# Optimization experiments

Measured on AMD Instinct MI355X. Metric: run time of the kernel, lower is better.

## Reference

```python
import jax, jax.numpy as jnp
import numpy as np


def setup_inputs() -> dict:
    key = jax.random.key(0)
    k0, k1, k2, k3, k4 = jax.random.split(key, 5)
    N, C, H, W, K = 16, 256, 32, 32, 4096
    inv = 1.0 / np.sqrt(C).astype(np.float32)
    latent = jax.random.normal(k0, (N, C, H, W), jnp.float32)
    codebook = jax.random.normal(k1, (K, C), jnp.float32) * inv
    wq = jax.random.normal(k2, (C, C), jnp.float32) * inv
    wk = jax.random.normal(k3, (C, C), jnp.float32) * inv
    wv = jax.random.normal(k4, (C, C), jnp.float32) * inv
    return {"latent": latent, "codebook": codebook, "wq": wq, "wk": wk, "wv": wv, "temperature": 1}


def reference(latent, codebook, wq, wk, wv, temperature):
    # deterministic=True, additionWeight=True, dropout=False
    # temperature >= 0 -> _gumbelAttention -> _softStraightThrough path
    assert temperature >= 0
    C = latent.shape[1]
    K = codebook.shape[0]
    scale = jnp.sqrt(jnp.asarray(C, jnp.float32))
    x = jnp.transpose(latent, (0, 2, 3, 1))          # [N,H,W,C]
    q = x @ wq.T                                      # nn.Linear: x @ W^T
    k = codebook @ wk.T                               # [K,C]
    v = codebook @ wv.T                               # [K,C]
    logit = jnp.einsum('nhwc,kc->nhwk', q, k) / scale  # [N,H,W,K]
    soft = jax.nn.softmax(logit, axis=-1)
    idx = jnp.argmax(logit, axis=-1)                  # [N,H,W]
    hard = jax.nn.one_hot(idx, K, dtype=jnp.float32)  # [N,H,W,K]
    soft_v = jnp.einsum('nhwk,kc->nhwc', soft, v)
    hard_v = jnp.einsum('nhwk,kc->nhwc', hard, v)
    # (hard - soft).detach() + soft  -> straight-through estimator
    result = jax.lax.stop_gradient(hard_v - soft_v) + soft_v
    quantized = jnp.transpose(result, (0, 3, 1, 2))   # [N,C,H,W]
    code = idx.astype(jnp.uint8)                      # sample.argmax(-1).byte()
    return (quantized, code, logit, v)
```

## Files before the change

### kernel.cpp

```cpp
#include <hip/hip_runtime.h>
#include <stdint.h>

typedef float f32x4 __attribute__((ext_vector_type(4)));
typedef short s16x8 __attribute__((ext_vector_type(8)));

#define QUANT_OFF 0
#define CODE_OFF  4194304
#define LOGIT_OFF 4210688
#define V_OFF     71319552

#define ARGMAX_MARGIN 0.0078125f

__device__ __forceinline__ unsigned short f2bf(float f) {
  unsigned int u = __float_as_uint(f);
  u = u + 0x7fffu + ((u >> 16) & 1u);
  return (unsigned short)(u >> 16);
}

__device__ __forceinline__ void load_lds16(const void* g, void* l) {
  __builtin_amdgcn_global_load_lds(
      (const __attribute__((address_space(1))) unsigned int*)g,
      (__attribute__((address_space(3))) unsigned int*)l, 16, 0, 0);
}

__global__ __launch_bounds__(256) void kvq_kernel(
    const float* __restrict__ latent, const float* __restrict__ wq,
    const float* __restrict__ cb, const float* __restrict__ wk, const float* __restrict__ wv,
    float* __restrict__ qf, unsigned short* __restrict__ qh,
    float* __restrict__ kf, unsigned short* __restrict__ kh, float* __restrict__ vout)
{
  __shared__ __align__(16) float A_s[2][2048];
  __shared__ __align__(16) float B_s[2][2048];
  const int t = threadIdx.x;
  const int bid = blockIdx.x;
  const int tx = t & 15;
  const int ry = t >> 4;

  if (bid >= 512) {
    const int qb = bid - 512;
    const int rowBase = (qb & 255) * 64;
    const int colBase = (qb >> 8) * 64;
    const int n = rowBase >> 10;
    const int hw0 = rowBase & 1023;
    float acc[4][4] = {{0.f}};

    #define QSTAGE(B, KT) do {                                                        \
      _Pragma("unroll")                                                               \
      for (int it = 0; it < 2; ++it) {                                                \
        int c = it * 256 + t;                                                         \
        int kk = c >> 4, rq = c & 15;                                                 \
        load_lds16(latent + ((size_t)(n * 256 + (KT) * 32 + kk) * 1024 + hw0 + rq * 4), \
                   &A_s[B][c * 4]);                                                   \
        int col = c >> 3, ls = c & 7;                                                 \
        int sk = ls ^ (col & 7);                                                      \
        load_lds16(wq + ((size_t)(colBase + col) * 256 + (KT) * 32 + sk * 4),          \
                   &B_s[B][c * 4]);                                                   \
      } } while (0)

    QSTAGE(0, 0);
    #pragma unroll 1
    for (int kt = 0; kt < 8; ++kt) {
      const int buf = kt & 1;
      __syncthreads();
      if (kt < 7) QSTAGE(buf ^ 1, kt + 1);
      const float* As = A_s[buf];
      const float* Bs = B_s[buf];
      #pragma unroll
      for (int kc = 0; kc < 8; ++kc) {
        f32x4 a[4], b[4];
        #pragma unroll
        for (int c = 0; c < 4; ++c) a[c] = *(const f32x4*)&As[(kc * 4 + c) * 64 + ry * 4];
        #pragma unroll
        for (int j = 0; j < 4; ++j) {
          const int col = tx + 16 * j;
          b[j] = *(const f32x4*)&Bs[col * 32 + (kc ^ (col & 7)) * 4];
        }
        #pragma unroll
        for (int i = 0; i < 4; ++i)
          #pragma unroll
          for (int j = 0; j < 4; ++j) {
            acc[i][j] = fmaf(a[0][i], b[j].x, acc[i][j]);
            acc[i][j] = fmaf(a[1][i], b[j].y, acc[i][j]);
            acc[i][j] = fmaf(a[2][i], b[j].z, acc[i][j]);
            acc[i][j] = fmaf(a[3][i], b[j].w, acc[i][j]);
          }
      }
    }
    #undef QSTAGE
    #pragma unroll
    for (int i = 0; i < 4; ++i) {
      const int r = rowBase + ry * 4 + i;
      #pragma unroll
      for (int j = 0; j < 4; ++j) {
        const int c = colBase + tx + 16 * j;
        qf[(size_t)r * 256 + c] = acc[i][j];
        qh[(size_t)r * 256 + c] = f2bf(acc[i][j] * 0.0625f);
      }
    }
  } else {
    const bool isV = bid >= 256;
    const int kb = bid & 255;
    const int rowBase = (kb & 63) * 64;
    const int colBase = (kb >> 6) * 64;
    const float* W = isV ? wv : wk;
    float acc[4][4] = {{0.f}};

    #define KSTAGE(B, KT) do {                                                        \
      _Pragma("unroll")                                                               \
      for (int it = 0; it < 2; ++it) {                                                \
        int c = it * 256 + t;                                                         \
        int row = c >> 3, ls = c & 7;                                                 \
        int sk = ls ^ (row & 7);                                                      \
        load_lds16(cb + ((size_t)(rowBase + row) * 256 + (KT) * 32 + sk * 4),          \
                   &A_s[B][c * 4]);                                                   \
        load_lds16(W  + ((size_t)(colBase + row) * 256 + (KT) * 32 + sk * 4),          \
                   &B_s[B][c * 4]);                                                   \
      } } while (0)

    KSTAGE(0, 0);
    #pragma unroll 1
    for (int kt = 0; kt < 8; ++kt) {
      const int buf = kt & 1;
      __syncthreads();
      if (kt < 7) KSTAGE(buf ^ 1, kt + 1);
      const float* As = A_s[buf];
      const float* Bs = B_s[buf];
      #pragma unroll
      for (int kc = 0; kc < 8; ++kc) {
        f32x4 a[4], b[4];
        #pragma unroll
        for (int i = 0; i < 4; ++i) {
          const int row = ry + 16 * i;
          a[i] = *(const f32x4*)&As[row * 32 + (kc ^ (row & 7)) * 4];
        }
        #pragma unroll
        for (int j = 0; j < 4; ++j) {
          const int col = tx + 16 * j;
          b[j] = *(const f32x4*)&Bs[col * 32 + (kc ^ (col & 7)) * 4];
        }
        #pragma unroll
        for (int i = 0; i < 4; ++i)
          #pragma unroll
          for (int j = 0; j < 4; ++j) {
            acc[i][j] = fmaf(a[i].x, b[j].x, acc[i][j]);
            acc[i][j] = fmaf(a[i].y, b[j].y, acc[i][j]);
            acc[i][j] = fmaf(a[i].z, b[j].z, acc[i][j]);
            acc[i][j] = fmaf(a[i].w, b[j].w, acc[i][j]);
          }
      }
    }
    #undef KSTAGE
    #pragma unroll
    for (int i = 0; i < 4; ++i) {
      const int r = rowBase + ry + 16 * i;
      #pragma unroll
      for (int j = 0; j < 4; ++j) {
        const int c = colBase + tx + 16 * j;
        if (isV) {
          vout[(size_t)r * 256 + c] = acc[i][j];
        } else {
          kf[(size_t)r * 256 + c] = acc[i][j];
          kh[(size_t)r * 256 + c] = f2bf(acc[i][j]);
        }
      }
    }
  }
}

__global__ __launch_bounds__(256) void logit_gemm(
    const unsigned short* __restrict__ qh, const unsigned short* __restrict__ kh,
    float* __restrict__ out, float* __restrict__ pmax)
{
  __shared__ short AsBuf[2][128 * 32];
  __shared__ short BsBuf[2][128 * 32];
  __shared__ float Pm[128][2];
  const int t = threadIdx.x;
  const int bid = blockIdx.x;
  const int wg = (bid & 7) * 512 + (bid >> 3);
  const int aRow0 = (wg >> 5) * 128;
  const int bRow0 = (wg & 31) * 128;
  const int lane = t & 63, wid = t >> 6;
  const int wr = wid >> 1, wc = wid & 1;
  f32x4 acc[4][4];
  #pragma unroll
  for (int m = 0; m < 4; ++m)
    #pragma unroll
    for (int n = 0; n < 4; ++n) { acc[m][n].x = 0.f; acc[m][n].y = 0.f; acc[m][n].z = 0.f; acc[m][n].w = 0.f; }

  const short* qs = (const short*)qh;
  const short* ks = (const short*)kh;

  #define STAGE32(AB, BB, KT) do {                                          \
    _Pragma("unroll")                                                       \
    for (int ci = 0; ci < 2; ++ci) {                                        \
      int c = ci * 256 + t;                                                 \
      int row = c >> 2;                                                     \
      int slot = (c & 3) ^ (row & 3);                                       \
      int koff = (KT) * 32 + slot * 8;                                      \
      load_lds16(qs + (size_t)(aRow0 + row) * 256 + koff, (AB) + c * 8);    \
      load_lds16(ks + (size_t)(bRow0 + row) * 256 + koff, (BB) + c * 8);    \
    } } while (0)

  STAGE32(AsBuf[0], BsBuf[0], 0);
  #pragma unroll
  for (int kt = 0; kt < 8; ++kt) {
    const int buf = kt & 1;
    __syncthreads();
    if (kt < 7) STAGE32(AsBuf[buf ^ 1], BsBuf[buf ^ 1], kt + 1);
    const short* As = AsBuf[buf];
    const short* Bs = BsBuf[buf];
    s16x8 af[4], bfr[4];
    #pragma unroll
    for (int m = 0; m < 4; ++m) {
      int row = wr * 64 + m * 16 + (lane & 15);
      int slot = (lane >> 4) ^ (row & 3);
      af[m] = *(const s16x8*)(As + row * 32 + slot * 8);
    }
    #pragma unroll
    for (int n = 0; n < 4; ++n) {
      int row = wc * 64 + n * 16 + (lane & 15);
      int slot = (lane >> 4) ^ (row & 3);
      bfr[n] = *(const s16x8*)(Bs + row * 32 + slot * 8);
    }
    #pragma unroll
    for (int m = 0; m < 4; ++m)
      #pragma unroll
      for (int n = 0; n < 4; ++n)
        acc[m][n] = __builtin_amdgcn_mfma_f32_16x16x32_bf16(af[m], bfr[n], acc[m][n], 0, 0, 0);
  }
  #undef STAGE32

  #pragma unroll
  for (int m = 0; m < 4; ++m)
    #pragma unroll
    for (int j = 0; j < 4; ++j) {
      float bm = fmaxf(fmaxf(acc[m][0][j], acc[m][1][j]),
                       fmaxf(acc[m][2][j], acc[m][3][j]));
      #pragma unroll
      for (int off = 1; off < 16; off <<= 1) bm = fmaxf(bm, __shfl_xor(bm, off));
      if ((lane & 15) == 0) Pm[wr * 64 + m * 16 + (lane >> 4) * 4 + j][wc] = bm;
    }
  const int colLane = lane & 15, rowQuad = (lane >> 4) * 4;
  #pragma unroll
  for (int m = 0; m < 4; ++m)
    #pragma unroll
    for (int n = 0; n < 4; ++n) {
      int row = aRow0 + wr * 64 + m * 16 + rowQuad;
      int col = bRow0 + wc * 64 + n * 16 + colLane;
      #pragma unroll
      for (int j = 0; j < 4; ++j)
        out[(size_t)(row + j) * 4096 + col] = acc[m][n][j];
    }
  __syncthreads();
  if (t < 128) pmax[(size_t)(aRow0 + t) * 32 + (bRow0 >> 7)] = fmaxf(Pm[t][0], Pm[t][1]);
}

__global__ __launch_bounds__(1024) void finalize_kernel(
    const float* __restrict__ logit, const float* __restrict__ pmax,
    const float* __restrict__ qf, const float* __restrict__ kf,
    const float* __restrict__ vout, float* __restrict__ quant, float* __restrict__ code)
{
  __shared__ __align__(16) float Vs[32][260];
  __shared__ int idxArr[32];
  const int t = threadIdx.x, wave = t >> 6, lane = t & 63;
  const int nh = blockIdx.x, n = nh >> 5, h = nh & 31;
  for (int ri = 0; ri < 2; ++ri) {
    const int w = wave * 2 + ri;
    const size_t r = (size_t)nh * 32 + w;
    float pv = -3e38f;
    if (lane < 32) pv = pmax[r * 32 + lane];
    float gmax = pv;
    #pragma unroll
    for (int off = 32; off; off >>= 1) gmax = fmaxf(gmax, __shfl_xor(gmax, off));
    const float thr = gmax - ARGMAX_MARGIN;
    const unsigned long long bmAll = __ballot(pv >= thr);
    int tot = 0, firstJ = 0x7fffffff;
    {
      unsigned long long bm = bmAll;
      #pragma unroll 1
      while (bm) {
        const int nb = __ffsll(bm) - 1; bm &= bm - 1;
        const float2 lv = *(const float2*)&logit[r * 4096 + nb * 128 + lane * 2];
        unsigned long long c0 = __ballot(lv.x >= thr);
        unsigned long long c1 = __ballot(lv.y >= thr);
        tot += __popcll(c0) + __popcll(c1);
        if (firstJ == 0x7fffffff && (c0 | c1)) {
          int j0 = c0 ? nb * 128 + 2 * (__ffsll(c0) - 1)     : 0x7fffffff;
          int j1 = c1 ? nb * 128 + 2 * (__ffsll(c1) - 1) + 1 : 0x7fffffff;
          firstJ = j0 < j1 ? j0 : j1;
        }
      }
    }
    int bestJ = firstJ;
    if (tot > 1) {
      const f32x4 qv = ((const f32x4*)(qf + r * 256))[lane];
      float bestV = -3e38f; bestJ = 0x7fffffff;
      unsigned long long bm = bmAll;
      #pragma unroll 1
      while (bm) {
        const int nb = __ffsll(bm) - 1; bm &= bm - 1;
        const float2 lv = *(const float2*)&logit[r * 4096 + nb * 128 + lane * 2];
        unsigned long long c0 = __ballot(lv.x >= thr);
        unsigned long long c1 = __ballot(lv.y >= thr);
        #pragma unroll 1
        for (int half = 0; half < 2; ++half) {
          unsigned long long mm = half ? c1 : c0;
          #pragma unroll 1
          while (mm) {
            const int L = __ffsll(mm) - 1; mm &= mm - 1;
            const int j = nb * 128 + L * 2 + half;
            const f32x4 kv = ((const f32x4*)(kf + (size_t)j * 256))[lane];
            double s = (double)qv.x * kv.x + (double)qv.y * kv.y
                     + (double)qv.z * kv.z + (double)qv.w * kv.w;
            #pragma unroll
            for (int off = 32; off; off >>= 1) s += __shfl_xor(s, off);
            const float val = (float)(s * 0.0625);
            if (val > bestV || (val == bestV && j < bestJ)) { bestV = val; bestJ = j; }
          }
        }
      }
    }
    if (lane == 0) idxArr[w] = bestJ;
  }
  __syncthreads();
  for (int ri = 0; ri < 2; ++ri) {
    const int w2 = wave * 2 + ri;
    const int idx = idxArr[w2];
    const f32x4 vv = ((const f32x4*)(vout + (size_t)idx * 256))[lane];
    *(f32x4*)&Vs[w2][lane * 4] = vv;
  }
  __syncthreads();
  const int wcol = t & 31, cg = t >> 5;
  #pragma unroll
  for (int cc = 0; cc < 8; ++cc) {
    const int c = cg * 8 + cc;
    quant[(((size_t)n * 256 + c) * 32 + h) * 32 + wcol] = Vs[wcol][c];
  }
  if (t < 32) code[nh * 32 + t] = (float)(idxArr[t] & 255);
}

extern "C" void kernel_launch(void* const* d_in, const int* in_sizes, int n_in,
                              void* d_out, int out_size, void* d_ws, size_t ws_size,
                              hipStream_t stream) {
  (void)in_sizes; (void)n_in; (void)out_size; (void)ws_size;
  const float* latent = (const float*)d_in[0];
  const float* cb     = (const float*)d_in[1];
  const float* wq     = (const float*)d_in[2];
  const float* wk     = (const float*)d_in[3];
  const float* wv     = (const float*)d_in[4];

  float* out   = (float*)d_out;
  float* quant = out + QUANT_OFF;
  float* code  = out + CODE_OFF;
  float* logit = out + LOGIT_OFF;
  float* vout  = out + V_OFF;

  char* ws = (char*)d_ws;
  float*          qf   = (float*)(ws + 0);
  float*          kf   = (float*)(ws + 16777216);
  unsigned short* qh   = (unsigned short*)(ws + 20971520);
  unsigned short* kh   = (unsigned short*)(ws + 29360128);
  float*          pmax = (float*)(ws + 31457280);

  kvq_kernel<<<1536, 256, 0, stream>>>(latent, wq, cb, wk, wv, qf, qh, kf, kh, vout);
  logit_gemm<<<4096, 256, 0, stream>>>(qh, kh, logit, pmax);
  finalize_kernel<<<512, 1024, 0, stream>>>(logit, pmax, qf, kf, vout, quant, code);
}
```

Measured before the change: 170.2 us.

## Enlarge projection GEMM tiles to 128x128 with 8x8 per-thread micro-tiles

The Q/K/V projection kernel now uses 128x128 output tiles with a K-step of 16 and 8x8 accumulators per thread, instead of 64x64 tiles with 4x4 accumulators. The grid shrinks from 1536 to 384 blocks and the LDS swizzle is adjusted to the 16-wide rows. The goal is more FMA work per LDS read and fewer redundant global loads. In exchange, register pressure rises (64 accumulators), fewer blocks are available to fill the CUs, and there are more sync steps per tile.

```diff
diff --git a/kernel.cpp b/kernel.cpp
--- a/kernel.cpp
+++ b/kernel.cpp
@@ -23,6 +23,7 @@
       (__attribute__((address_space(3))) unsigned int*)l, 16, 0, 0);
 }
 
+#define SWZ4(x) (((x) ^ ((x) >> 3)) & 3)
 __global__ __launch_bounds__(256) void kvq_kernel(
     const float* __restrict__ latent, const float* __restrict__ wq,
     const float* __restrict__ cb, const float* __restrict__ wk, const float* __restrict__ wv,
@@ -36,112 +37,115 @@
   const int tx = t & 15;
   const int ry = t >> 4;
 
-  if (bid >= 512) {
-    const int qb = bid - 512;
-    const int rowBase = (qb & 255) * 64;
-    const int colBase = (qb >> 8) * 64;
+  if (bid >= 128) {
+    const int qb = bid - 128;
+    const int rowBase = (qb >> 1) * 128;
+    const int colBase = (qb & 1) * 128;
     const int n = rowBase >> 10;
     const int hw0 = rowBase & 1023;
-    float acc[4][4] = {{0.f}};
-
-    #define QSTAGE(B, KT) do {                                                        \
-      _Pragma("unroll")                                                               \
-      for (int it = 0; it < 2; ++it) {                                                \
-        int c = it * 256 + t;                                                         \
-        int kk = c >> 4, rq = c & 15;                                                 \
-        load_lds16(latent + ((size_t)(n * 256 + (KT) * 32 + kk) * 1024 + hw0 + rq * 4), \
-                   &A_s[B][c * 4]);                                                   \
-        int col = c >> 3, ls = c & 7;                                                 \
-        int sk = ls ^ (col & 7);                                                      \
-        load_lds16(wq + ((size_t)(colBase + col) * 256 + (KT) * 32 + sk * 4),          \
-                   &B_s[B][c * 4]);                                                   \
+    float acc[8][8] = {};
+
+    #define QSTAGE(B, KT) do {                                                          \
+      _Pragma("unroll")                                                                 \
+      for (int it = 0; it < 2; ++it) {                                                  \
+        int c = it * 256 + t;                                                           \
+        int kk = c >> 5, rq = c & 31;                                                   \
+        load_lds16(latent + ((size_t)(n * 256 + (KT) * 16 + kk) * 1024 + hw0 + rq * 4), \
+                   &A_s[B][c * 4]);                                                     \
+        int col = c >> 2, ls = c & 3;                                                   \
+        int sk = ls ^ SWZ4(col);                                                        \
+        load_lds16(wq + ((size_t)(colBase + col) * 256 + (KT) * 16 + sk * 4),           \
+                   &B_s[B][c * 4]);                                                     \
       } } while (0)
 
     QSTAGE(0, 0);
     #pragma unroll 1
-    for (int kt = 0; kt < 8; ++kt) {
+    for (int kt = 0; kt < 16; ++kt) {
       const int buf = kt & 1;
       __syncthreads();
-      if (kt < 7) QSTAGE(buf ^ 1, kt + 1);
+      if (kt < 15) QSTAGE(buf ^ 1, kt + 1);
       const float* As = A_s[buf];
       const float* Bs = B_s[buf];
       #pragma unroll
-      for (int kc = 0; kc < 8; ++kc) {
-        f32x4 a[4], b[4];
-        #pragma unroll
-        for (int c = 0; c < 4; ++c) a[c] = *(const f32x4*)&As[(kc * 4 + c) * 64 + ry * 4];
-        #pragma unroll
-        for (int j = 0; j < 4; ++j) {
+      for (int kc = 0; kc < 4; ++kc) {
+        f32x4 alo[4], ahi[4], b[8];
+        #pragma unroll
+        for (int k4 = 0; k4 < 4; ++k4) {
+          alo[k4] = *(const f32x4*)&As[(kc * 4 + k4) * 128 + ry * 8];
+          ahi[k4] = *(const f32x4*)&As[(kc * 4 + k4) * 128 + ry * 8 + 4];
+        }
+        #pragma unroll
+        for (int j = 0; j < 8; ++j) {
           const int col = tx + 16 * j;
-          b[j] = *(const f32x4*)&Bs[col * 32 + (kc ^ (col & 7)) * 4];
-        }
-        #pragma unroll
-        for (int i = 0; i < 4; ++i)
+          b[j] = *(const f32x4*)&Bs[col * 16 + (kc ^ SWZ4(col)) * 4];
+        }
+        #pragma unroll
+        for (int k4 = 0; k4 < 4; ++k4)
           #pragma unroll
-          for (int j = 0; j < 4; ++j) {
-            acc[i][j] = fmaf(a[0][i], b[j].x, acc[i][j]);
-            acc[i][j] = fmaf(a[1][i], b[j].y, acc[i][j]);
-            acc[i][j] = fmaf(a[2][i], b[j].z, acc[i][j]);
-            acc[i][j] = fmaf(a[3][i], b[j].w, acc[i][j]);
+          for (int i = 0; i < 8; ++i) {
+            const float av = (i < 4) ? alo[k4][i] : ahi[k4][i - 4];
+            #pragma unroll
+            for (int j = 0; j < 8; ++j)
+              acc[i][j] = fmaf(av, b[j][k4], acc[i][j]);
           }
       }
     }
     #undef QSTAGE
     #pragma unroll
-    for (int i = 0; i < 4; ++i) {
-      const int r = rowBase + ry * 4 + i;
-      #pragma unroll
-      for (int j = 0; j < 4; ++j) {
+    for (int i = 0; i < 8; ++i) {
+      const int r = rowBase + ry * 8 + i;
+      #pragma unroll
+      for (int j = 0; j < 8; ++j) {
         const int c = colBase + tx + 16 * j;
         qf[(size_t)r * 256 + c] = acc[i][j];
         qh[(size_t)r * 256 + c] = f2bf(acc[i][j] * 0.0625f);
       }
     }
   } else {
-    const bool isV = bid >= 256;
-    const int kb = bid & 255;
-    const int rowBase = (kb & 63) * 64;
-    const int colBase = (kb >> 6) * 64;
+    const bool isV = bid >= 64;
+    const int kb = bid & 63;
+    const int rowBase = (kb >> 1) * 128;
+    const int colBase = (kb & 1) * 128;
     const float* W = isV ? wv : wk;
-    float acc[4][4] = {{0.f}};
-
-    #define KSTAGE(B, KT) do {                                                        \
-      _Pragma("unroll")                                                               \
-      for (int it = 0; it < 2; ++it) {                                                \
-        int c = it * 256 + t;                                                         \
-        int row = c >> 3, ls = c & 7;                                                 \
-        int sk = ls ^ (row & 7);                                                      \
-        load_lds16(cb + ((size_t)(rowBase + row) * 256 + (KT) * 32 + sk * 4),          \
-                   &A_s[B][c * 4]);                                                   \
-        load_lds16(W  + ((size_t)(colBase + row) * 256 + (KT) * 32 + sk * 4),          \
-                   &B_s[B][c * 4]);                                                   \
+    float acc[8][8] = {};
+
+    #define KSTAGE(B, KT) do {                                                          \
+      _Pragma("unroll")                                                                 \
+      for (int it = 0; it < 2; ++it) {                                                  \
+        int c = it * 256 + t;                                                           \
+        int rw = c >> 2, ls = c & 3;                                                    \
+        int sk = ls ^ SWZ4(rw);                                                         \
+        load_lds16(cb + ((size_t)(rowBase + rw) * 256 + (KT) * 16 + sk * 4),            \
+                   &A_s[B][c * 4]);                                                     \
+        load_lds16(W  + ((size_t)(colBase + rw) * 256 + (KT) * 16 + sk * 4),            \
+                   &B_s[B][c * 4]);                                                     \
       } } while (0)
 
     KSTAGE(0, 0);
     #pragma unroll 1
-    for (int kt = 0; kt < 8; ++kt) {
+    for (int kt = 0; kt < 16; ++kt) {
       const int buf = kt & 1;
       __syncthreads();
-      if (kt < 7) KSTAGE(buf ^ 1, kt + 1);
+      if (kt < 15) KSTAGE(buf ^ 1, kt + 1);
       const float* As = A_s[buf];
       const float* Bs = B_s[buf];
       #pragma unroll
-      for (int kc = 0; kc < 8; ++kc) {
-        f32x4 a[4], b[4];
-        #pragma unroll
-        for (int i = 0; i < 4; ++i) {
-          const int row = ry + 16 * i;
-          a[i] = *(const f32x4*)&As[row * 32 + (kc ^ (row & 7)) * 4];
-        }
-        #pragma unroll
-        for (int j = 0; j < 4; ++j) {
+      for (int kc = 0; kc < 4; ++kc) {
+        f32x4 a[8], b[8];
+        #pragma unroll
+        for (int i = 0; i < 8; ++i) {
+          const int row = ry * 8 + i;
+          a[i] = *(const f32x4*)&As[row * 16 + (kc ^ SWZ4(row)) * 4];
+        }
+        #pragma unroll
+        for (int j = 0; j < 8; ++j) {
           const int col = tx + 16 * j;
-          b[j] = *(const f32x4*)&Bs[col * 32 + (kc ^ (col & 7)) * 4];
-        }
-        #pragma unroll
-        for (int i = 0; i < 4; ++i)
+          b[j] = *(const f32x4*)&Bs[col * 16 + (kc ^ SWZ4(col)) * 4];
+        }
+        #pragma unroll
+        for (int i = 0; i < 8; ++i)
           #pragma unroll
-          for (int j = 0; j < 4; ++j) {
+          for (int j = 0; j < 8; ++j) {
             acc[i][j] = fmaf(a[i].x, b[j].x, acc[i][j]);
             acc[i][j] = fmaf(a[i].y, b[j].y, acc[i][j]);
             acc[i][j] = fmaf(a[i].z, b[j].z, acc[i][j]);
@@ -151,10 +155,10 @@
     }
     #undef KSTAGE
     #pragma unroll
-    for (int i = 0; i < 4; ++i) {
-      const int r = rowBase + ry + 16 * i;
-      #pragma unroll
-      for (int j = 0; j < 4; ++j) {
+    for (int i = 0; i < 8; ++i) {
+      const int r = rowBase + ry * 8 + i;
+      #pragma unroll
+      for (int j = 0; j < 8; ++j) {
         const int c = colBase + tx + 16 * j;
         if (isV) {
           vout[(size_t)r * 256 + c] = acc[i][j];
@@ -362,7 +366,7 @@
   unsigned short* kh   = (unsigned short*)(ws + 29360128);
   float*          pmax = (float*)(ws + 31457280);
 
-  kvq_kernel<<<1536, 256, 0, stream>>>(latent, wq, cb, wk, wv, qf, qh, kf, kh, vout);
+  kvq_kernel<<<384, 256, 0, stream>>>(latent, wq, cb, wk, wv, qf, qh, kf, kh, vout);
   logit_gemm<<<4096, 256, 0, stream>>>(qh, kh, logit, pmax);
   finalize_kernel<<<512, 1024, 0, stream>>>(logit, pmax, qf, kf, vout, quant, code);
 }
```

New measurement: 198.4 us. 1.17x slower.
